# Performance work log

Hardware: AMD Instinct MI355X
Metric: run time of the kernel (lower is better)

Reference implementation:

```python
import jax, jax.numpy as jnp
import numpy as np

IN_FEATURES = 4096
OUT_FEATURES = 11008
BATCH = 2048


def setup_inputs() -> dict:
    key = jax.random.key(0)
    k1, k2, k3, k4 = jax.random.split(key, 4)
    # int8-range activations, stored as int32 for exact integer accumulation
    input = jax.random.randint(k1, (BATCH, IN_FEATURES), -127, 128, dtype=jnp.int32)
    # ternary weights in {-1, 0, 1}
    ternary_weight = jax.random.randint(k2, (OUT_FEATURES, IN_FEATURES), -1, 2, dtype=jnp.int32)
    weight_scale = jax.random.uniform(k3, (OUT_FEATURES, 1), dtype=jnp.float32, minval=0.01, maxval=0.1)
    bias = jax.random.normal(k4, (OUT_FEATURES,), dtype=jnp.float32) * 0.01
    return {"input": input, "ternary_weight": ternary_weight,
            "weight_scale": weight_scale, "bias": bias}


def reference(input, ternary_weight, weight_scale, bias):
    # Equivalent to the per-column add/sub loop: int32 accumulate of
    # input @ ternary_weight.T, since w in {-1,0,1}.
    acc = jnp.einsum('bi,oi->bo', input, ternary_weight)  # int32 [B, O]
    out = acc.astype(jnp.float32) * weight_scale.reshape(1, -1)
    out = out + bias
    return out
```

## Files before the change

### kernel.cpp

```cpp
#include <hip/hip_runtime.h>
#include <stdint.h>

#define BATCH   2048
#define KDIM    4096
#define NDIM    11008

#define BM 128
#define BN 128
#define BK 128
#define NT (KDIM / BK)
#define ABYTES (BM * BK)
#define BBYTES (BN * BK)
#define BUF_BYTES (ABYTES + BBYTES)
#define A_OFF 0
#define B_OFF ABYTES

typedef __attribute__((ext_vector_type(4))) int i32x4;

typedef const __attribute__((address_space(1))) char glob_char;
typedef __attribute__((address_space(3))) char lds_char;

__device__ __forceinline__ unsigned pack4(i32x4 v) {
  return  ((unsigned)v.x & 0xFFu)
        | (((unsigned)v.y & 0xFFu) << 8)
        | (((unsigned)v.z & 0xFFu) << 16)
        | (((unsigned)v.w)         << 24);
}

__global__ __launch_bounds__(256) void convert_i32_i8(const int* __restrict__ src,
                                                      unsigned* __restrict__ dst,
                                                      int n4) {
  int idx = blockIdx.x * 256 + threadIdx.x;
  if (idx >= n4) return;
  i32x4 v = ((const i32x4*)src)[idx];
  dst[idx] = pack4(v);
}

__global__ __launch_bounds__(256, 2) void ternary_gemm(const char* __restrict__ A8,
                                                       const char* __restrict__ B8,
                                                       const float* __restrict__ scale,
                                                       const float* __restrict__ bias,
                                                       float* __restrict__ out) {
  __shared__ char lds[2 * BUF_BYTES];

  const int tid  = threadIdx.x;
  const int wid  = tid >> 6;
  const int lane = tid & 63;

  const int nwg = gridDim.x;
  const int cpx = nwg >> 3;
  const int wg  = (blockIdx.x & 7) * cpx + (blockIdx.x >> 3);
  const int mt = wg & 15;
  const int nt = wg >> 4;
  const int arow0 = mt * BM;
  const int brow0 = nt * BN;

  const int wr = wid >> 1;
  const int wc = wid & 1;
  const int rsub = lane & 15;
  const int sgrp = lane >> 4;

  const int srow  = tid >> 3;
  const int sslot = (tid & 7) ^ (srow & 7);
  const char* gA[4];
  const char* gB[4];
#pragma unroll
  for (int r = 0; r < 4; ++r) {
    gA[r] = A8 + (size_t)(arow0 + r * 32 + srow) * KDIM + sslot * 16;
    gB[r] = B8 + (size_t)(brow0 + r * 32 + srow) * KDIM + sslot * 16;
  }

  auto stage = [&](const char* g, int bufo, int dsto) {
    __builtin_amdgcn_global_load_lds((glob_char*)g,
        (lds_char*)(lds + bufo + dsto + wid * 1024), 16, 0, 0);
  };

  int offA[4][2], offB[4][2];
#pragma unroll
  for (int m = 0; m < 4; ++m) {
    const int row = wr * 64 + m * 16 + rsub;
#pragma unroll
    for (int ks = 0; ks < 2; ++ks) {
      const int p = (ks * 4 + sgrp) ^ (row & 7);
      offA[m][ks] = A_OFF + row * 128 + p * 16;
    }
  }
#pragma unroll
  for (int n = 0; n < 4; ++n) {
    const int row = wc * 64 + n * 16 + rsub;
#pragma unroll
    for (int ks = 0; ks < 2; ++ks) {
      const int p = (ks * 4 + sgrp) ^ (row & 7);
      offB[n][ks] = B_OFF + row * 128 + p * 16;
    }
  }

  i32x4 acc[4][4];
#pragma unroll
  for (int m = 0; m < 4; ++m)
#pragma unroll
    for (int n = 0; n < 4; ++n)
      acc[m][n] = (i32x4){0, 0, 0, 0};

  int cur = 0, nxt = BUF_BYTES;

#pragma unroll
  for (int r = 0; r < 4; ++r) stage(gA[r], cur, A_OFF + r * 4096);
#pragma unroll
  for (int r = 0; r < 4; ++r) stage(gB[r], cur, B_OFF + r * 4096);
  asm volatile("s_waitcnt vmcnt(0)" ::: "memory");
  __builtin_amdgcn_s_barrier();

  for (int t = 0; t < NT; ++t) {
    const int ktn = ((t + 1 < NT) ? t + 1 : NT - 1) * BK;

#pragma unroll
    for (int r = 0; r < 4; ++r) stage(gA[r] + ktn, nxt, A_OFF + r * 4096);
#pragma unroll
    for (int r = 0; r < 4; ++r) stage(gB[r] + ktn, nxt, B_OFF + r * 4096);

    {
      i32x4 a0 = *(const i32x4*)(lds + cur + offA[0][0]);
      i32x4 a1 = *(const i32x4*)(lds + cur + offA[1][0]);
      i32x4 a2 = *(const i32x4*)(lds + cur + offA[2][0]);
      i32x4 a3 = *(const i32x4*)(lds + cur + offA[3][0]);
      i32x4 b0 = *(const i32x4*)(lds + cur + offB[0][0]);
      i32x4 b1 = *(const i32x4*)(lds + cur + offB[1][0]);
      i32x4 b2 = *(const i32x4*)(lds + cur + offB[2][0]);
      i32x4 b3 = *(const i32x4*)(lds + cur + offB[3][0]);
      __builtin_amdgcn_s_setprio(1);
      acc[0][0] = __builtin_amdgcn_mfma_i32_16x16x64_i8(a0, b0, acc[0][0], 0, 0, 0);
      acc[1][0] = __builtin_amdgcn_mfma_i32_16x16x64_i8(a1, b0, acc[1][0], 0, 0, 0);
      acc[2][0] = __builtin_amdgcn_mfma_i32_16x16x64_i8(a2, b0, acc[2][0], 0, 0, 0);
      acc[3][0] = __builtin_amdgcn_mfma_i32_16x16x64_i8(a3, b0, acc[3][0], 0, 0, 0);
      acc[0][1] = __builtin_amdgcn_mfma_i32_16x16x64_i8(a0, b1, acc[0][1], 0, 0, 0);
      acc[1][1] = __builtin_amdgcn_mfma_i32_16x16x64_i8(a1, b1, acc[1][1], 0, 0, 0);
      acc[2][1] = __builtin_amdgcn_mfma_i32_16x16x64_i8(a2, b1, acc[2][1], 0, 0, 0);
      acc[3][1] = __builtin_amdgcn_mfma_i32_16x16x64_i8(a3, b1, acc[3][1], 0, 0, 0);
      acc[0][2] = __builtin_amdgcn_mfma_i32_16x16x64_i8(a0, b2, acc[0][2], 0, 0, 0);
      acc[1][2] = __builtin_amdgcn_mfma_i32_16x16x64_i8(a1, b2, acc[1][2], 0, 0, 0);
      acc[2][2] = __builtin_amdgcn_mfma_i32_16x16x64_i8(a2, b2, acc[2][2], 0, 0, 0);
      acc[3][2] = __builtin_amdgcn_mfma_i32_16x16x64_i8(a3, b2, acc[3][2], 0, 0, 0);
      acc[0][3] = __builtin_amdgcn_mfma_i32_16x16x64_i8(a0, b3, acc[0][3], 0, 0, 0);
      acc[1][3] = __builtin_amdgcn_mfma_i32_16x16x64_i8(a1, b3, acc[1][3], 0, 0, 0);
      acc[2][3] = __builtin_amdgcn_mfma_i32_16x16x64_i8(a2, b3, acc[2][3], 0, 0, 0);
      acc[3][3] = __builtin_amdgcn_mfma_i32_16x16x64_i8(a3, b3, acc[3][3], 0, 0, 0);
      __builtin_amdgcn_s_setprio(0);
    }

    {
      i32x4 a0 = *(const i32x4*)(lds + cur + offA[0][1]);
      i32x4 a1 = *(const i32x4*)(lds + cur + offA[1][1]);
      i32x4 a2 = *(const i32x4*)(lds + cur + offA[2][1]);
      i32x4 a3 = *(const i32x4*)(lds + cur + offA[3][1]);
      i32x4 b0 = *(const i32x4*)(lds + cur + offB[0][1]);
      i32x4 b1 = *(const i32x4*)(lds + cur + offB[1][1]);
      i32x4 b2 = *(const i32x4*)(lds + cur + offB[2][1]);
      i32x4 b3 = *(const i32x4*)(lds + cur + offB[3][1]);
      __builtin_amdgcn_s_setprio(1);
      acc[0][0] = __builtin_amdgcn_mfma_i32_16x16x64_i8(a0, b0, acc[0][0], 0, 0, 0);
      acc[1][0] = __builtin_amdgcn_mfma_i32_16x16x64_i8(a1, b0, acc[1][0], 0, 0, 0);
      acc[2][0] = __builtin_amdgcn_mfma_i32_16x16x64_i8(a2, b0, acc[2][0], 0, 0, 0);
      acc[3][0] = __builtin_amdgcn_mfma_i32_16x16x64_i8(a3, b0, acc[3][0], 0, 0, 0);
      acc[0][1] = __builtin_amdgcn_mfma_i32_16x16x64_i8(a0, b1, acc[0][1], 0, 0, 0);
      acc[1][1] = __builtin_amdgcn_mfma_i32_16x16x64_i8(a1, b1, acc[1][1], 0, 0, 0);
      acc[2][1] = __builtin_amdgcn_mfma_i32_16x16x64_i8(a2, b1, acc[2][1], 0, 0, 0);
      acc[3][1] = __builtin_amdgcn_mfma_i32_16x16x64_i8(a3, b1, acc[3][1], 0, 0, 0);
      acc[0][2] = __builtin_amdgcn_mfma_i32_16x16x64_i8(a0, b2, acc[0][2], 0, 0, 0);
      acc[1][2] = __builtin_amdgcn_mfma_i32_16x16x64_i8(a1, b2, acc[1][2], 0, 0, 0);
      acc[2][2] = __builtin_amdgcn_mfma_i32_16x16x64_i8(a2, b2, acc[2][2], 0, 0, 0);
      acc[3][2] = __builtin_amdgcn_mfma_i32_16x16x64_i8(a3, b2, acc[3][2], 0, 0, 0);
      acc[0][3] = __builtin_amdgcn_mfma_i32_16x16x64_i8(a0, b3, acc[0][3], 0, 0, 0);
      acc[1][3] = __builtin_amdgcn_mfma_i32_16x16x64_i8(a1, b3, acc[1][3], 0, 0, 0);
      acc[2][3] = __builtin_amdgcn_mfma_i32_16x16x64_i8(a2, b3, acc[2][3], 0, 0, 0);
      acc[3][3] = __builtin_amdgcn_mfma_i32_16x16x64_i8(a3, b3, acc[3][3], 0, 0, 0);
      __builtin_amdgcn_s_setprio(0);
    }

    asm volatile("s_waitcnt vmcnt(0)" ::: "memory");
    __builtin_amdgcn_s_barrier();

    const int tb = cur; cur = nxt; nxt = tb;
  }

  const int crow = sgrp * 4;
#pragma unroll
  for (int n = 0; n < 4; ++n) {
    const int col = brow0 + wc * 64 + n * 16 + rsub;
    const float sc = scale[col];
    const float bs = bias[col];
#pragma unroll
    for (int m = 0; m < 4; ++m) {
      const int r0 = arow0 + wr * 64 + m * 16 + crow;
#pragma unroll
      for (int j = 0; j < 4; ++j) {
        out[(size_t)(r0 + j) * NDIM + col] = (float)acc[m][n][j] * sc + bs;
      }
    }
  }
}

extern "C" void kernel_launch(void* const* d_in, const int* in_sizes, int n_in,
                              void* d_out, int out_size, void* d_ws, size_t ws_size,
                              hipStream_t stream) {
  const int*   input  = (const int*)d_in[0];
  const int*   weight = (const int*)d_in[1];
  const float* scale  = (const float*)d_in[2];
  const float* bias   = (const float*)d_in[3];
  float*       out    = (float*)d_out;

  const size_t needA = (size_t)BATCH * KDIM;
  const size_t needB = (size_t)NDIM * KDIM;

  char* A8 = (char*)d_ws;
  char* B8 = A8 + needA;
  const int nA4 = (int)(needA / 4);
  const int nB4 = (int)(needB / 4);
  convert_i32_i8<<<(nA4 + 255) / 256, 256, 0, stream>>>(input, (unsigned*)A8, nA4);
  convert_i32_i8<<<(nB4 + 255) / 256, 256, 0, stream>>>(weight, (unsigned*)B8, nB4);

  const dim3 grid((BATCH / BM) * (NDIM / BN));
  const dim3 block(256);
  ternary_gemm<<<grid, block, 0, stream>>>(A8, B8, scale, bias, out);
  (void)ws_size; (void)n_in; (void)in_sizes; (void)out_size;
}
```

Before: 150.1 us.

## Pack ternary weights to 2 bits and decode in-register before int8 MFMA

Replaces the int8 weight conversion with a 2-bit packing kernel, so each weight tile staged into LDS is a quarter of its former size and is expanded to int8 in registers with bit tricks before the MFMAs. This is meant to cut global and LDS traffic for the weight operand and the workspace write in the conversion pass. The smaller LDS footprint is paired with a request for three workgroups per CU instead of two, and the tile ordering is changed so groups of four M tiles share an N tile. The cost is extra ALU decode work per MFMA group, plus possible register pressure under the tighter launch bound.

```diff
diff --git a/kernel.cpp b/kernel.cpp
--- a/kernel.cpp
+++ b/kernel.cpp
@@ -10,10 +10,11 @@
 #define BK 128
 #define NT (KDIM / BK)
 #define ABYTES (BM * BK)
-#define BBYTES (BN * BK)
+#define BBYTES (BN * BK / 4)
 #define BUF_BYTES (ABYTES + BBYTES)
 #define A_OFF 0
 #define B_OFF ABYTES
+#define BPK_ROWB 1024
 
 typedef __attribute__((ext_vector_type(4))) int i32x4;
 
@@ -36,8 +37,35 @@
   dst[idx] = pack4(v);
 }
 
-__global__ __launch_bounds__(256, 2) void ternary_gemm(const char* __restrict__ A8,
-                                                       const char* __restrict__ B8,
+__global__ __launch_bounds__(256) void convert_w2(const int* __restrict__ src,
+                                                  unsigned* __restrict__ dst) {
+  const int f = blockIdx.x * 256 + threadIdx.x;
+  const int r = f >> 8;
+  const int i = f & 255;
+  const int* p = src + (size_t)r * KDIM + i * 16;
+  unsigned w = 0;
+#pragma unroll
+  for (int e = 0; e < 16; ++e) {
+    const unsigned v = (unsigned)p[e] & 3u;
+    w |= v << (8 * (e & 3) + 2 * (e >> 2));
+  }
+  const int slot = (i & 7) ^ (r & 7);
+  dst[(size_t)r * 256 + (i >> 3) * 8 + slot] = w;
+}
+
+__device__ __forceinline__ i32x4 dec2(unsigned w) {
+  const unsigned M1 = 0x01010101u, M2 = 0x02020202u;
+  i32x4 r;
+  unsigned x;
+  x = w;      r.x = (int)((x & M1) | ((x & M2) * 0x7Fu));
+  x = w >> 2; r.y = (int)((x & M1) | ((x & M2) * 0x7Fu));
+  x = w >> 4; r.z = (int)((x & M1) | ((x & M2) * 0x7Fu));
+  x = w >> 6; r.w = (int)((x & M1) | ((x & M2) * 0x7Fu));
+  return r;
+}
+
+__global__ __launch_bounds__(256, 3) void ternary_gemm(const char* __restrict__ A8,
+                                                       const unsigned* __restrict__ B2,
                                                        const float* __restrict__ scale,
                                                        const float* __restrict__ bias,
                                                        float* __restrict__ out) {
@@ -47,11 +75,11 @@
   const int wid  = tid >> 6;
   const int lane = tid & 63;
 
-  const int nwg = gridDim.x;
-  const int cpx = nwg >> 3;
-  const int wg  = (blockIdx.x & 7) * cpx + (blockIdx.x >> 3);
-  const int mt = wg & 15;
-  const int nt = wg >> 4;
+  const int wg  = (blockIdx.x & 7) * 172 + (blockIdx.x >> 3);
+  const int mtq = wg / 344;
+  const int r   = wg - mtq * 344;
+  const int nt  = r >> 2;
+  const int mt  = mtq * 4 + (r & 3);
   const int arow0 = mt * BM;
   const int brow0 = nt * BN;
 
@@ -60,19 +88,21 @@
   const int rsub = lane & 15;
   const int sgrp = lane >> 4;
 
-  const int srow  = tid >> 3;
-  const int sslot = (tid & 7) ^ (srow & 7);
-  const char* gA[4];
-  const char* gB[4];
-#pragma unroll
-  for (int r = 0; r < 4; ++r) {
-    gA[r] = A8 + (size_t)(arow0 + r * 32 + srow) * KDIM + sslot * 16;
-    gB[r] = B8 + (size_t)(brow0 + r * 32 + srow) * KDIM + sslot * 16;
-  }
-
-  auto stage = [&](const char* g, int bufo, int dsto) {
-    __builtin_amdgcn_global_load_lds((glob_char*)g,
-        (lds_char*)(lds + bufo + dsto + wid * 1024), 16, 0, 0);
+  const int srowA = tid >> 3;
+  const int slotA = (tid & 7) ^ (srowA & 7);
+  const int srowB = tid >> 1;
+  const int shalfB = (tid & 1) * 16;
+
+  auto stage_tile = [&](int bufo, int kt) {
+#pragma unroll
+    for (int rr = 0; rr < 4; ++rr) {
+      __builtin_amdgcn_global_load_lds(
+          (glob_char*)(A8 + (size_t)(arow0 + rr * 32 + srowA) * KDIM + kt * BK + slotA * 16),
+          (lds_char*)(lds + bufo + A_OFF + rr * 4096 + wid * 1024), 16, 0, 0);
+    }
+    __builtin_amdgcn_global_load_lds(
+        (glob_char*)((const char*)B2 + (size_t)(brow0 + srowB) * BPK_ROWB + kt * (BK / 4) + shalfB),
+        (lds_char*)(lds + bufo + B_OFF + wid * 1024), 16, 0, 0);
   };
 
   int offA[4][2], offB[4][2];
@@ -91,7 +121,7 @@
 #pragma unroll
     for (int ks = 0; ks < 2; ++ks) {
       const int p = (ks * 4 + sgrp) ^ (row & 7);
-      offB[n][ks] = B_OFF + row * 128 + p * 16;
+      offB[n][ks] = B_OFF + row * 32 + p * 4;
     }
   }
 
@@ -104,30 +134,29 @@
 
   int cur = 0, nxt = BUF_BYTES;
 
-#pragma unroll
-  for (int r = 0; r < 4; ++r) stage(gA[r], cur, A_OFF + r * 4096);
-#pragma unroll
-  for (int r = 0; r < 4; ++r) stage(gB[r], cur, B_OFF + r * 4096);
+  stage_tile(cur, 0);
   asm volatile("s_waitcnt vmcnt(0)" ::: "memory");
   __builtin_amdgcn_s_barrier();
 
   for (int t = 0; t < NT; ++t) {
-    const int ktn = ((t + 1 < NT) ? t + 1 : NT - 1) * BK;
-
-#pragma unroll
-    for (int r = 0; r < 4; ++r) stage(gA[r] + ktn, nxt, A_OFF + r * 4096);
-#pragma unroll
-    for (int r = 0; r < 4; ++r) stage(gB[r] + ktn, nxt, B_OFF + r * 4096);
-
-    {
-      i32x4 a0 = *(const i32x4*)(lds + cur + offA[0][0]);
-      i32x4 a1 = *(const i32x4*)(lds + cur + offA[1][0]);
-      i32x4 a2 = *(const i32x4*)(lds + cur + offA[2][0]);
-      i32x4 a3 = *(const i32x4*)(lds + cur + offA[3][0]);
-      i32x4 b0 = *(const i32x4*)(lds + cur + offB[0][0]);
-      i32x4 b1 = *(const i32x4*)(lds + cur + offB[1][0]);
-      i32x4 b2 = *(const i32x4*)(lds + cur + offB[2][0]);
-      i32x4 b3 = *(const i32x4*)(lds + cur + offB[3][0]);
+    const int kt1 = (t + 1 < NT) ? t + 1 : NT - 1;
+
+    stage_tile(nxt, kt1);
+
+#pragma unroll
+    for (int ks = 0; ks < 2; ++ks) {
+      i32x4 a0 = *(const i32x4*)(lds + cur + offA[0][ks]);
+      i32x4 a1 = *(const i32x4*)(lds + cur + offA[1][ks]);
+      i32x4 a2 = *(const i32x4*)(lds + cur + offA[2][ks]);
+      i32x4 a3 = *(const i32x4*)(lds + cur + offA[3][ks]);
+      unsigned w0 = *(const unsigned*)(lds + cur + offB[0][ks]);
+      unsigned w1 = *(const unsigned*)(lds + cur + offB[1][ks]);
+      unsigned w2 = *(const unsigned*)(lds + cur + offB[2][ks]);
+      unsigned w3 = *(const unsigned*)(lds + cur + offB[3][ks]);
+      i32x4 b0 = dec2(w0);
+      i32x4 b1 = dec2(w1);
+      i32x4 b2 = dec2(w2);
+      i32x4 b3 = dec2(w3);
       __builtin_amdgcn_s_setprio(1);
       acc[0][0] = __builtin_amdgcn_mfma_i32_16x16x64_i8(a0, b0, acc[0][0], 0, 0, 0);
       acc[1][0] = __builtin_amdgcn_mfma_i32_16x16x64_i8(a1, b0, acc[1][0], 0, 0, 0);
@@ -148,35 +177,6 @@
       __builtin_amdgcn_s_setprio(0);
     }
 
-    {
-      i32x4 a0 = *(const i32x4*)(lds + cur + offA[0][1]);
-      i32x4 a1 = *(const i32x4*)(lds + cur + offA[1][1]);
-      i32x4 a2 = *(const i32x4*)(lds + cur + offA[2][1]);
-      i32x4 a3 = *(const i32x4*)(lds + cur + offA[3][1]);
-      i32x4 b0 = *(const i32x4*)(lds + cur + offB[0][1]);
-      i32x4 b1 = *(const i32x4*)(lds + cur + offB[1][1]);
-      i32x4 b2 = *(const i32x4*)(lds + cur + offB[2][1]);
-      i32x4 b3 = *(const i32x4*)(lds + cur + offB[3][1]);
-      __builtin_amdgcn_s_setprio(1);
-      acc[0][0] = __builtin_amdgcn_mfma_i32_16x16x64_i8(a0, b0, acc[0][0], 0, 0, 0);
-      acc[1][0] = __builtin_amdgcn_mfma_i32_16x16x64_i8(a1, b0, acc[1][0], 0, 0, 0);
-      acc[2][0] = __builtin_amdgcn_mfma_i32_16x16x64_i8(a2, b0, acc[2][0], 0, 0, 0);
-      acc[3][0] = __builtin_amdgcn_mfma_i32_16x16x64_i8(a3, b0, acc[3][0], 0, 0, 0);
-      acc[0][1] = __builtin_amdgcn_mfma_i32_16x16x64_i8(a0, b1, acc[0][1], 0, 0, 0);
-      acc[1][1] = __builtin_amdgcn_mfma_i32_16x16x64_i8(a1, b1, acc[1][1], 0, 0, 0);
-      acc[2][1] = __builtin_amdgcn_mfma_i32_16x16x64_i8(a2, b1, acc[2][1], 0, 0, 0);
-      acc[3][1] = __builtin_amdgcn_mfma_i32_16x16x64_i8(a3, b1, acc[3][1], 0, 0, 0);
-      acc[0][2] = __builtin_amdgcn_mfma_i32_16x16x64_i8(a0, b2, acc[0][2], 0, 0, 0);
-      acc[1][2] = __builtin_amdgcn_mfma_i32_16x16x64_i8(a1, b2, acc[1][2], 0, 0, 0);
-      acc[2][2] = __builtin_amdgcn_mfma_i32_16x16x64_i8(a2, b2, acc[2][2], 0, 0, 0);
-      acc[3][2] = __builtin_amdgcn_mfma_i32_16x16x64_i8(a3, b2, acc[3][2], 0, 0, 0);
-      acc[0][3] = __builtin_amdgcn_mfma_i32_16x16x64_i8(a0, b3, acc[0][3], 0, 0, 0);
-      acc[1][3] = __builtin_amdgcn_mfma_i32_16x16x64_i8(a1, b3, acc[1][3], 0, 0, 0);
-      acc[2][3] = __builtin_amdgcn_mfma_i32_16x16x64_i8(a2, b3, acc[2][3], 0, 0, 0);
-      acc[3][3] = __builtin_amdgcn_mfma_i32_16x16x64_i8(a3, b3, acc[3][3], 0, 0, 0);
-      __builtin_amdgcn_s_setprio(0);
-    }
-
     asm volatile("s_waitcnt vmcnt(0)" ::: "memory");
     __builtin_amdgcn_s_barrier();
 
@@ -210,17 +210,16 @@
   float*       out    = (float*)d_out;
 
   const size_t needA = (size_t)BATCH * KDIM;
-  const size_t needB = (size_t)NDIM * KDIM;
-
-  char* A8 = (char*)d_ws;
-  char* B8 = A8 + needA;
+  const size_t needB = (size_t)NDIM * BPK_ROWB;
+
+  char*     A8  = (char*)d_ws;
+  unsigned* Bpk = (unsigned*)(A8 + needA);
   const int nA4 = (int)(needA / 4);
-  const int nB4 = (int)(needB / 4);
   convert_i32_i8<<<(nA4 + 255) / 256, 256, 0, stream>>>(input, (unsigned*)A8, nA4);
-  convert_i32_i8<<<(nB4 + 255) / 256, 256, 0, stream>>>(weight, (unsigned*)B8, nB4);
+  convert_w2<<<NDIM * (KDIM / 16) / 256, 256, 0, stream>>>(weight, Bpk);
 
   const dim3 grid((BATCH / BM) * (NDIM / BN));
   const dim3 block(256);
-  ternary_gemm<<<grid, block, 0, stream>>>(A8, B8, scale, bias, out);
-  (void)ws_size; (void)n_in; (void)in_sizes; (void)out_size;
-}
+  ternary_gemm<<<grid, block, 0, stream>>>(A8, Bpk, scale, bias, out);
+  (void)ws_size; (void)n_in; (void)in_sizes; (void)out_size; (void)needB;
+}
```

New measurement: 147.9 us. Within noise of the previous version (-1.4%).
